# Kernel optimization log

Measured on AMD Instinct MI355X. Metric: run time of the kernel, lower is better.

## Reference

```python
import jax, jax.numpy as jnp
import numpy as np

B, CE = 2, 32
D, H, W = 12, 256, 256
PATCH = (5, 19, 19)
DWS = (1, 2, 2)            # patch_dws_fact
REAL = (5, 38, 38)          # patch_size * dws
STRIDE = (1, 9, 9)
OFF = (0, 2, 2)             # fixed random-crop offsets (max_random_crop=(0,5,5))
NPT = (8, 25, 25)           # nb_patches per dim after crop
HID = 256
EPS = 1e-6


def setup_inputs() -> dict:
    key = jax.random.key(0)
    k1, k2, k3, k4, k5 = jax.random.split(key, 5)
    gt = jax.random.randint(k1, (B, 1, D, H, W), 0, 50).astype(jnp.float32)
    affs = (jax.random.uniform(k2, (B, 3, D, H, W)) < 0.9).astype(jnp.float32)
    target = jnp.concatenate([gt, affs], axis=1)            # [B,4,D,H,W]
    pred = jax.random.normal(k3, (B, CE, D, H, W), dtype=jnp.float32)
    W1 = jax.random.normal(k4, (CE, HID), dtype=jnp.float32) * 0.1
    b1 = jnp.zeros((HID,), jnp.float32)
    W2 = jax.random.normal(k5, (HID, PATCH[0] * PATCH[1] * PATCH[2]), dtype=jnp.float32) * 0.05
    b2 = jnp.zeros((PATCH[0] * PATCH[1] * PATCH[2],), jnp.float32)
    return {"target": target, "pred": pred, "W1": W1, "b1": b1, "W2": W2, "b2": b2}


def _extract_patches(x, shp, strd, npt):
    # x: [N,C,D,H,W] -> [N*nd*nh*nw, C, *shp], torch-unfold ordering (N-major, then d,h,w)
    N, C = x.shape[:2]
    di = jnp.arange(npt[0])[:, None] * strd[0] + jnp.arange(shp[0])  # [nd,pd]
    hi = jnp.arange(npt[1])[:, None] * strd[1] + jnp.arange(shp[1])
    wi = jnp.arange(npt[2])[:, None] * strd[2] + jnp.arange(shp[2])
    p = x[:, :, di]                     # [N,C,nd,pd,H,W]
    p = p[:, :, :, :, hi]               # [N,C,nd,pd,nh,ph,W]
    p = p[:, :, :, :, :, :, wi]         # [N,C,nd,pd,nh,ph,nw,pw]
    p = jnp.transpose(p, (0, 2, 4, 6, 1, 3, 5, 7))
    return p.reshape(N * npt[0] * npt[1] * npt[2], C, *shp)


def _strided_centers(x, start, strd, npt):
    # shape-(1,1,1) patch extraction == strided slice, flattened in (N,d,h,w) order
    c = x[:, :, start[0]::strd[0], start[1]::strd[1], start[2]::strd[2]]
    c = c[:, :, :npt[0], :npt[1], :npt[2]]
    return jnp.transpose(c, (0, 2, 3, 4, 1))  # [N,nd,nh,nw,C]


def reference(target, pred, W1, b1, W2, b2):
    gt = target[:, :1]                                    # GT segmentation labels
    bmask = jnp.max(1.0 - target[:, 1:], axis=1, keepdims=True)  # boundary mask

    # crop_slice_targets with fixed offsets OFF
    gt_c = gt[:, :, OFF[0]:, OFF[1]:, OFF[2]:]
    gt_patches = _extract_patches(gt_c, REAL, STRIDE, NPT)  # [Np,1,5,38,38]
    Np = gt_patches.shape[0]

    # crop_slice_emb: start shifted by real_patch//2
    emb_start = tuple(o + r // 2 for o, r in zip(OFF, REAL))  # (2,21,21)
    centers = _strided_centers(gt, emb_start, STRIDE, NPT).reshape(Np)        # label at center
    on_bnd = _strided_centers(bmask, emb_start, STRIDE, NPT).reshape(Np)

    me_masks = (gt_patches != centers[:, None, None, None, None]).astype(jnp.float32)
    ignore = (gt_patches == 0).astype(jnp.float32)

    # MaxPool3d(kernel=stride=DWS): [Np,1,5,38,38] -> [Np,1,5,19,19]
    def pool(t):
        t = t.reshape(Np, 1, REAL[0] // DWS[0], DWS[0], PATCH[1], DWS[1], PATCH[2], DWS[2])
        return t.max(axis=(3, 5, 7))
    patch_targets = pool(me_masks)
    patch_ignore = pool(ignore) > 0

    valid = (centers != 0) & (on_bnd != 1.0)              # [Np]

    # pred embeddings: pred_dws_fact=1 so same crop/stride; 1x1x1 patches
    emb = _strided_centers(pred, emb_start, STRIDE, NPT).reshape(Np, CE)
    h = jax.nn.relu(emb @ W1 + b1)
    pred_patches = jax.nn.sigmoid(h @ W2 + b2).reshape(Np, 1, *PATCH)

    # exclusion of invalid patches == zeroing both operands in the Dice sums;
    # ignore-mask voxels are zeroed in pred and target as in the original
    m = (valid[:, None, None, None, None] & (~patch_ignore)).astype(jnp.float32)
    p = pred_patches * m
    t = patch_targets * m

    # SorensenDiceLoss (single channel): -2 * sum(p*t) / (sum(p^2)+sum(t^2))
    num = jnp.sum(p * t)
    den = jnp.sum(p * p) + jnp.sum(t * t)
    loss = -2.0 * num / jnp.maximum(den, EPS)
    return loss
```

## Files before the change

kernel.cpp:

```cpp
#include <hip/hip_runtime.h>

#define B_    2
#define CE_   32
#define D_    12
#define H_    256
#define W_    256
#define HW_   (H_*W_)
#define HID_  256
#define NPD   8
#define NPH   25
#define NPW   25
#define NP_   10000
#define PJ    1805
#define NTILE 113
#define JTP   114
#define MS_   16
#define MB_   157
#define NSLOT (MB_*64)

typedef __attribute__((ext_vector_type(8))) short s8v;
typedef __attribute__((ext_vector_type(4))) float f32x4;

__device__ __forceinline__ unsigned short f2bf(float f) {
    unsigned u = __float_as_uint(f);
    u += 0x7FFFu + ((u >> 16) & 1u);
    return (unsigned short)(u >> 16);
}

__device__ __forceinline__ void decompose_n(int n, int& b, int& pd, int& ph, int& pw) {
    b = n / (NPD*NPH*NPW);
    int r = n - b*(NPD*NPH*NPW);
    pd = r / (NPH*NPW);
    int r2 = r - pd*(NPH*NPW);
    ph = r2 / NPW;
    pw = r2 - ph*NPW;
}

__global__ __launch_bounds__(256) void k_stage(
    const float* __restrict__ W2, const float* __restrict__ b2,
    const float* __restrict__ target, const float* __restrict__ pred,
    const float* __restrict__ W1, const float* __restrict__ b1,
    unsigned short* __restrict__ W2t, int2* __restrict__ lut,
    unsigned short* __restrict__ M, unsigned short* __restrict__ hA,
    int2* __restrict__ meta, int* __restrict__ cnt)
{
    const int bx = blockIdx.x;
    const int t  = threadIdx.x;

    if (bx < 114) {
        __shared__ unsigned short tile[16][264];
        const int j0 = bx * 16;
        const int jj = t & 15, kb = t >> 4;
        #pragma unroll
        for (int ki = 0; ki < 16; ki++) {
            const int k = kb*16 + ki;
            const int j = j0 + jj;
            const float v = (j < PJ) ? W2[(size_t)k*PJ + j] : 0.f;
            tile[jj][k] = f2bf(v);
        }
        __syncthreads();
        const int jr = t >> 4, kc = t & 15;
        s8v a = *(const s8v*)&tile[jr][kc*16];
        s8v b = *(const s8v*)&tile[jr][kc*16+8];
        *(s8v*)&W2t[(size_t)(j0+jr)*HID_ + kc*16]     = a;
        *(s8v*)&W2t[(size_t)(j0+jr)*HID_ + kc*16 + 8] = b;
    } else if (bx == 114) {
        for (int i = t; i < JTP*16; i += 256) {
            int off = 0; float bj = 0.f;
            if (i < PJ) {
                const int dz = i/361, rj = i - dz*361;
                const int yy = rj/19, xx = rj - yy*19;
                off = dz*HW_ + yy*(2*W_) + xx*2;
                bj = b2[i];
            }
            lut[i] = make_int2(off, __float_as_int(bj));
        }
    } else if (bx < 1651) {
        __shared__ float rows[5][256];
        const int bx2 = bx - 115;
        const int bd = bx2 >> 6;
        const int h0 = (bx2 & 63) << 2;
        const int b  = bd / D_, d = bd - b*D_;
        const size_t gbase = ((size_t)(b*4*D_) + d)*HW_;
        #pragma unroll
        for (int r = 0; r < 5; r++) {
            int h = h0 + r; if (h > 255) h = 255;
            rows[r][t] = target[gbase + h*W_ + t];
        }
        __syncthreads();
        const int w1 = (t < 255) ? t+1 : 255;
        #pragma unroll
        for (int r = 0; r < 4; r++) {
            const float g00 = rows[r][t],   g01 = rows[r][w1];
            const float g10 = rows[r+1][t], g11 = rows[r+1][w1];
            const float mn = fminf(fminf(g00,g01), fminf(g10,g11));
            const float mx = fmaxf(fmaxf(g00,g01), fmaxf(g10,g11));
            M[(size_t)bd*HW_ + (h0+r)*W_ + t] = (unsigned short)(((int)mn << 8) | (int)mx);
        }
    } else {
        __shared__ float emb_s[64][36];
        __shared__ int   slot_s[64];
        const int pb = bx - 1651;
        const int n0 = pb * 64;
        {
            const int m = t & 63, cg = t >> 6;
            int n = n0 + m; if (n >= NP_) n = NP_-1;
            int b, pd, ph, pw; decompose_n(n, b, pd, ph, pw);
            const int dc = 2+pd, hc = 21+9*ph, wc = 21+9*pw;
            const size_t base = ((size_t)(b*CE_ + cg*8)*D_ + dc)*HW_ + (size_t)hc*W_ + wc;
            #pragma unroll
            for (int i = 0; i < 8; i++)
                emb_s[m][cg*8+i] = pred[base + (size_t)i*D_*HW_];
        }
        if (t < 64) {
            int n = n0 + t; const bool inb = (n < NP_); if (!inb) n = NP_-1;
            int b, pd, ph, pw; decompose_n(n, b, pd, ph, pw);
            const int dc = 2+pd, hc = 21+9*ph, wc = 21+9*pw;
            const size_t tb = ((size_t)(b*4)*D_ + dc)*HW_ + (size_t)hc*W_ + wc;
            const float ctr = target[tb];
            const float a1 = target[tb + (size_t)(1*D_*HW_)];
            const float a2 = target[tb + (size_t)(2*D_*HW_)];
            const float a3 = target[tb + (size_t)(3*D_*HW_)];
            const bool v = inb && (ctr!=0.f) && (a1!=0.f) && (a2!=0.f) && (a3!=0.f);
            const unsigned long long bal = __ballot(v);
            int base = 0;
            if (t == 0) base = atomicAdd(cnt, __popcll(bal));
            base = __shfl(base, 0);
            int s = -1;
            if (v) {
                s = base + (int)__popcll(bal & ((1ull << t) - 1ull));
                const int ci = (int)ctr;
                meta[s] = make_int2((b*D_+pd)*HW_ + (2+9*ph)*W_ + (2+9*pw),
                                    (ci<<8)|ci);
            }
            slot_s[t] = s;
        }
        __syncthreads();
        float wcol[CE_];
        #pragma unroll
        for (int i = 0; i < CE_; i++) wcol[i] = W1[(size_t)i*HID_ + t];
        const float bb = b1[t];
        const int kk = t>>5, quad = (t>>3)&3, e = t&7;
        for (int mm = 0; mm < 64; mm++) {
            const int s = slot_s[mm];
            if (s < 0) continue;
            float a = bb;
            #pragma unroll
            for (int cc = 0; cc < CE_; cc += 4) {
                const float4 ev = *(const float4*)&emb_s[mm][cc];
                a = fmaf(ev.x, wcol[cc+0], a);
                a = fmaf(ev.y, wcol[cc+1], a);
                a = fmaf(ev.z, wcol[cc+2], a);
                a = fmaf(ev.w, wcol[cc+3], a);
            }
            hA[(size_t)(((s>>4)*8+kk)*4+quad)*128 + (s&15)*8 + e] = f2bf(fmaxf(a, 0.f));
        }
    }
}

__global__ __launch_bounds__(256, 4) void k_main(
    const unsigned short* __restrict__ hA, const unsigned short* __restrict__ W2t,
    const int2* __restrict__ lut, const unsigned short* __restrict__ M,
    const int2* __restrict__ meta, const int* __restrict__ cnt,
    double* __restrict__ accs)
{
    __shared__ float red_s[4][3];
    const int tid  = threadIdx.x;
    const int wv   = tid >> 6;
    const int lane = tid & 63;
    const int quad = lane >> 4;
    const int l16  = lane & 15;
    const int jt0  = blockIdx.x * 2;
    const int ms   = blockIdx.y;
    const int nv   = *cnt;
    const int nmt  = (nv + 15) >> 4;

    s8v bfr0[8], bfr1[8];
    {
        const unsigned short* w0 = W2t + (size_t)(jt0*16 + l16)*HID_ + quad*8;
        const unsigned short* w1 = w0 + 16*HID_;
        #pragma unroll
        for (int kk = 0; kk < 8; kk++) {
            bfr0[kk] = *(const s8v*)(w0 + kk*32);
            bfr1[kk] = *(const s8v*)(w1 + kk*32);
        }
    }
    const int j0 = jt0*16 + l16, j1 = j0 + 16;
    const int2 lb0 = lut[j0], lb1 = lut[j1];
    const bool jok0 = (j0 < PJ), jok1 = (j1 < PJ);
    const float bj0 = __int_as_float(lb0.y), bj1 = __int_as_float(lb1.y);

    float num = 0.f, denp = 0.f, dent = 0.f;

    for (int mt = ms*4 + wv; mt < nmt; mt += MS_*4) {
        const unsigned short* arow = hA + (size_t)mt*4096 + quad*128 + l16*8;
        f32x4 a0 = {0.f,0.f,0.f,0.f}, a1 = {0.f,0.f,0.f,0.f};
        #pragma unroll
        for (int kk = 0; kk < 8; kk++) {
            const s8v af = *(const s8v*)(arow + kk*512);
            a0 = __builtin_amdgcn_mfma_f32_16x16x32_bf16(af, bfr0[kk], a0, 0, 0, 0);
            a1 = __builtin_amdgcn_mfma_f32_16x16x32_bf16(af, bfr1[kk], a1, 0, 0, 0);
        }
        #pragma unroll
        for (int r = 0; r < 4; r++) {
            const int p = mt*16 + quad*4 + r;
            const bool pok = (p < nv);
            const int2 md = meta[pok ? p : 0];
            const int mb = md.x;
            const unsigned cpv = (unsigned)md.y;
            if (pok) {
                if (jok0) {
                    const unsigned mv = M[mb + lb0.x];
                    if (mv >= 256u) {
                        const float tv = (mv != cpv) ? 1.f : 0.f;
                        const float pv = 1.f / (1.f + __expf(-(a0[r] + bj0)));
                        num  = fmaf(pv, tv, num);
                        denp = fmaf(pv, pv, denp);
                        dent += tv;
                    }
                }
                if (jok1) {
                    const unsigned mv = M[mb + lb1.x];
                    if (mv >= 256u) {
                        const float tv = (mv != cpv) ? 1.f : 0.f;
                        const float pv = 1.f / (1.f + __expf(-(a1[r] + bj1)));
                        num  = fmaf(pv, tv, num);
                        denp = fmaf(pv, pv, denp);
                        dent += tv;
                    }
                }
            }
        }
    }

    #pragma unroll
    for (int off = 32; off > 0; off >>= 1) {
        num  += __shfl_down(num,  off);
        denp += __shfl_down(denp, off);
        dent += __shfl_down(dent, off);
    }
    if (lane == 0) { red_s[wv][0] = num; red_s[wv][1] = denp; red_s[wv][2] = dent; }
    __syncthreads();
    if (tid == 0) {
        const float n_ = red_s[0][0]+red_s[1][0]+red_s[2][0]+red_s[3][0];
        const float p_ = red_s[0][1]+red_s[1][1]+red_s[2][1]+red_s[3][1];
        const float t_ = red_s[0][2]+red_s[1][2]+red_s[2][2]+red_s[3][2];
        const int slot = (blockIdx.x + blockIdx.y*57) & 31;
        atomicAdd(&accs[slot*4 + 0], (double)n_);
        atomicAdd(&accs[slot*4 + 1], (double)p_);
        atomicAdd(&accs[slot*4 + 2], (double)t_);
    }
}

__global__ void k_final(const double* __restrict__ accs, float* __restrict__ out) {
    double num = 0.0, den = 0.0;
    for (int s = 0; s < 32; s++) {
        num += accs[s*4 + 0];
        den += accs[s*4 + 1] + accs[s*4 + 2];
    }
    const double d = den > 1e-6 ? den : 1e-6;
    out[0] = (float)(-2.0 * num / d);
}

extern "C" void kernel_launch(void* const* d_in, const int* in_sizes, int n_in,
                              void* d_out, int out_size, void* d_ws, size_t ws_size,
                              hipStream_t stream) {
    const float* target = (const float*)d_in[0];
    const float* pred   = (const float*)d_in[1];
    const float* W1     = (const float*)d_in[2];
    const float* b1     = (const float*)d_in[3];
    const float* W2     = (const float*)d_in[4];
    const float* b2     = (const float*)d_in[5];
    float* out = (float*)d_out;

    char* ws = (char*)d_ws;
    double*         accs = (double*)ws;
    int*            cnt  = (int*)(ws + 1024);
    int2*           meta = (int2*)(ws + 1056);
    unsigned short* hA   = (unsigned short*)(ws + 81472);
    unsigned short* W2t  = (unsigned short*)(ws + 5226048);
    int2*           lut  = (int2*)(ws + 6159936);
    unsigned short* Mx   = (unsigned short*)(ws + 6174528);

    hipMemsetAsync(d_ws, 0, 1056, stream);
    hipLaunchKernelGGL(k_stage, dim3(1808),     dim3(256), 0, stream,
                       W2, b2, target, pred, W1, b1, W2t, lut, Mx, hA, meta, cnt);
    hipLaunchKernelGGL(k_main,  dim3(57, MS_),  dim3(256), 0, stream,
                       hA, W2t, lut, Mx, meta, cnt, accs);
    hipLaunchKernelGGL(k_final, dim3(1), dim3(1), 0, stream, accs, out);
}
```

Before: 313.9 us.

## Fuse final reduction into main kernel and reorder staging blocks

```diff
diff --git a/kernel.cpp b/kernel.cpp
--- a/kernel.cpp
+++ b/kernel.cpp
@@ -12,11 +12,9 @@
 #define NPW   25
 #define NP_   10000
 #define PJ    1805
-#define NTILE 113
 #define JTP   114
 #define MS_   16
-#define MB_   157
-#define NSLOT (MB_*64)
+#define PB_   313
 
 typedef __attribute__((ext_vector_type(8))) short s8v;
 typedef __attribute__((ext_vector_type(4))) float f32x4;
@@ -47,81 +45,30 @@
     const int bx = blockIdx.x;
     const int t  = threadIdx.x;
 
-    if (bx < 114) {
-        __shared__ unsigned short tile[16][264];
-        const int j0 = bx * 16;
-        const int jj = t & 15, kb = t >> 4;
-        #pragma unroll
-        for (int ki = 0; ki < 16; ki++) {
-            const int k = kb*16 + ki;
-            const int j = j0 + jj;
-            const float v = (j < PJ) ? W2[(size_t)k*PJ + j] : 0.f;
-            tile[jj][k] = f2bf(v);
-        }
-        __syncthreads();
-        const int jr = t >> 4, kc = t & 15;
-        s8v a = *(const s8v*)&tile[jr][kc*16];
-        s8v b = *(const s8v*)&tile[jr][kc*16+8];
-        *(s8v*)&W2t[(size_t)(j0+jr)*HID_ + kc*16]     = a;
-        *(s8v*)&W2t[(size_t)(j0+jr)*HID_ + kc*16 + 8] = b;
-    } else if (bx == 114) {
-        for (int i = t; i < JTP*16; i += 256) {
-            int off = 0; float bj = 0.f;
-            if (i < PJ) {
-                const int dz = i/361, rj = i - dz*361;
-                const int yy = rj/19, xx = rj - yy*19;
-                off = dz*HW_ + yy*(2*W_) + xx*2;
-                bj = b2[i];
-            }
-            lut[i] = make_int2(off, __float_as_int(bj));
-        }
-    } else if (bx < 1651) {
-        __shared__ float rows[5][256];
-        const int bx2 = bx - 115;
-        const int bd = bx2 >> 6;
-        const int h0 = (bx2 & 63) << 2;
-        const int b  = bd / D_, d = bd - b*D_;
-        const size_t gbase = ((size_t)(b*4*D_) + d)*HW_;
-        #pragma unroll
-        for (int r = 0; r < 5; r++) {
-            int h = h0 + r; if (h > 255) h = 255;
-            rows[r][t] = target[gbase + h*W_ + t];
-        }
-        __syncthreads();
-        const int w1 = (t < 255) ? t+1 : 255;
-        #pragma unroll
-        for (int r = 0; r < 4; r++) {
-            const float g00 = rows[r][t],   g01 = rows[r][w1];
-            const float g10 = rows[r+1][t], g11 = rows[r+1][w1];
-            const float mn = fminf(fminf(g00,g01), fminf(g10,g11));
-            const float mx = fmaxf(fmaxf(g00,g01), fmaxf(g10,g11));
-            M[(size_t)bd*HW_ + (h0+r)*W_ + t] = (unsigned short)(((int)mn << 8) | (int)mx);
-        }
-    } else {
-        __shared__ float emb_s[64][36];
-        __shared__ int   slot_s[64];
-        const int pb = bx - 1651;
-        const int n0 = pb * 64;
+    if (bx < PB_) {
+        __shared__ float emb_s[32][36];
+        __shared__ int   slot_s[32];
+        const int n0 = bx * 32;
         {
-            const int m = t & 63, cg = t >> 6;
+            const int m = t & 31, cg = t >> 5;
             int n = n0 + m; if (n >= NP_) n = NP_-1;
             int b, pd, ph, pw; decompose_n(n, b, pd, ph, pw);
             const int dc = 2+pd, hc = 21+9*ph, wc = 21+9*pw;
-            const size_t base = ((size_t)(b*CE_ + cg*8)*D_ + dc)*HW_ + (size_t)hc*W_ + wc;
+            const size_t base = ((size_t)(b*CE_ + cg*4)*D_ + dc)*HW_ + (size_t)hc*W_ + wc;
             #pragma unroll
-            for (int i = 0; i < 8; i++)
-                emb_s[m][cg*8+i] = pred[base + (size_t)i*D_*HW_];
-        }
-        if (t < 64) {
+            for (int i = 0; i < 4; i++)
+                emb_s[m][cg*4+i] = pred[base + (size_t)i*D_*HW_];
+        }
+        if (t < 32) {
             int n = n0 + t; const bool inb = (n < NP_); if (!inb) n = NP_-1;
             int b, pd, ph, pw; decompose_n(n, b, pd, ph, pw);
             const int dc = 2+pd, hc = 21+9*ph, wc = 21+9*pw;
             const size_t tb = ((size_t)(b*4)*D_ + dc)*HW_ + (size_t)hc*W_ + wc;
             const float ctr = target[tb];
-            const float a1 = target[tb + (size_t)(1*D_*HW_)];
-            const float a2 = target[tb + (size_t)(2*D_*HW_)];
-            const float a3 = target[tb + (size_t)(3*D_*HW_)];
-            const bool v = inb && (ctr!=0.f) && (a1!=0.f) && (a2!=0.f) && (a3!=0.f);
+            const float a1v = target[tb + (size_t)(1*D_*HW_)];
+            const float a2v = target[tb + (size_t)(2*D_*HW_)];
+            const float a3v = target[tb + (size_t)(3*D_*HW_)];
+            const bool v = inb && (ctr!=0.f) && (a1v!=0.f) && (a2v!=0.f) && (a3v!=0.f);
             const unsigned long long bal = __ballot(v);
             int base = 0;
             if (t == 0) base = atomicAdd(cnt, __popcll(bal));
@@ -141,7 +88,7 @@
         for (int i = 0; i < CE_; i++) wcol[i] = W1[(size_t)i*HID_ + t];
         const float bb = b1[t];
         const int kk = t>>5, quad = (t>>3)&3, e = t&7;
-        for (int mm = 0; mm < 64; mm++) {
+        for (int mm = 0; mm < 32; mm++) {
             const int s = slot_s[mm];
             if (s < 0) continue;
             float a = bb;
@@ -155,6 +102,56 @@
             }
             hA[(size_t)(((s>>4)*8+kk)*4+quad)*128 + (s&15)*8 + e] = f2bf(fmaxf(a, 0.f));
         }
+    } else if (bx < PB_ + JTP) {
+        __shared__ unsigned short tile[16][264];
+        const int j0 = (bx - PB_) * 16;
+        const int jj = t & 15, kb = t >> 4;
+        #pragma unroll
+        for (int ki = 0; ki < 16; ki++) {
+            const int k = kb*16 + ki;
+            const int j = j0 + jj;
+            const float v = (j < PJ) ? W2[(size_t)k*PJ + j] : 0.f;
+            tile[jj][k] = f2bf(v);
+        }
+        __syncthreads();
+        const int jr = t >> 4, kc = t & 15;
+        s8v a = *(const s8v*)&tile[jr][kc*16];
+        s8v b = *(const s8v*)&tile[jr][kc*16+8];
+        *(s8v*)&W2t[(size_t)(j0+jr)*HID_ + kc*16]     = a;
+        *(s8v*)&W2t[(size_t)(j0+jr)*HID_ + kc*16 + 8] = b;
+    } else if (bx == PB_ + JTP) {
+        for (int i = t; i < JTP*16; i += 256) {
+            int off = 0; float bj = 0.f;
+            if (i < PJ) {
+                const int dz = i/361, rj = i - dz*361;
+                const int yy = rj/19, xx = rj - yy*19;
+                off = dz*HW_ + yy*(2*W_) + xx*2;
+                bj = b2[i];
+            }
+            lut[i] = make_int2(off, __float_as_int(bj));
+        }
+    } else {
+        __shared__ float rows[9][256];
+        const int bx2 = bx - (PB_ + JTP + 1);
+        const int bd = bx2 >> 5;
+        const int h0 = (bx2 & 31) << 3;
+        const int b  = bd / D_, d = bd - b*D_;
+        const size_t gbase = ((size_t)(b*4*D_) + d)*HW_;
+        #pragma unroll
+        for (int r = 0; r < 9; r++) {
+            int h = h0 + r; if (h > 255) h = 255;
+            rows[r][t] = target[gbase + h*W_ + t];
+        }
+        __syncthreads();
+        const int w1 = (t < 255) ? t+1 : 255;
+        #pragma unroll
+        for (int r = 0; r < 8; r++) {
+            const float g00 = rows[r][t],   g01 = rows[r][w1];
+            const float g10 = rows[r+1][t], g11 = rows[r+1][w1];
+            const float mn = fminf(fminf(g00,g01), fminf(g10,g11));
+            const float mx = fmaxf(fmaxf(g00,g01), fmaxf(g10,g11));
+            M[(size_t)bd*HW_ + (h0+r)*W_ + t] = (unsigned short)(((int)mn << 8) | (int)mx);
+        }
     }
 }
 
@@ -162,7 +159,8 @@
     const unsigned short* __restrict__ hA, const unsigned short* __restrict__ W2t,
     const int2* __restrict__ lut, const unsigned short* __restrict__ M,
     const int2* __restrict__ meta, const int* __restrict__ cnt,
-    double* __restrict__ accs)
+    double* __restrict__ accs, unsigned* __restrict__ ticket,
+    float* __restrict__ out)
 {
     __shared__ float red_s[4][3];
     const int tid  = threadIdx.x;
@@ -189,8 +187,33 @@
     const int2 lb0 = lut[j0], lb1 = lut[j1];
     const bool jok0 = (j0 < PJ), jok1 = (j1 < PJ);
     const float bj0 = __int_as_float(lb0.y), bj1 = __int_as_float(lb1.y);
+    const unsigned short* Mp0 = M + lb0.x;
+    const unsigned short* Mp1 = M + lb1.x;
 
     float num = 0.f, denp = 0.f, dent = 0.f;
+
+#define EPI(MB, CPV) do {                                              \
+        if (jok0) {                                                    \
+            const unsigned mv = Mp0[(MB)];                             \
+            if (mv >= 256u) {                                          \
+                const float tv = (mv != (CPV)) ? 1.f : 0.f;            \
+                const float pv = 1.f / (1.f + __expf(-(a0[r] + bj0))); \
+                num  = fmaf(pv, tv, num);                              \
+                denp = fmaf(pv, pv, denp);                             \
+                dent += tv;                                            \
+            }                                                          \
+        }                                                              \
+        if (jok1) {                                                    \
+            const unsigned mv = Mp1[(MB)];                             \
+            if (mv >= 256u) {                                          \
+                const float tv = (mv != (CPV)) ? 1.f : 0.f;            \
+                const float pv = 1.f / (1.f + __expf(-(a1[r] + bj1))); \
+                num  = fmaf(pv, tv, num);                              \
+                denp = fmaf(pv, pv, denp);                             \
+                dent += tv;                                            \
+            }                                                          \
+        }                                                              \
+    } while (0)
 
     for (int mt = ms*4 + wv; mt < nmt; mt += MS_*4) {
         const unsigned short* arow = hA + (size_t)mt*4096 + quad*128 + l16*8;
@@ -201,37 +224,29 @@
             a0 = __builtin_amdgcn_mfma_f32_16x16x32_bf16(af, bfr0[kk], a0, 0, 0, 0);
             a1 = __builtin_amdgcn_mfma_f32_16x16x32_bf16(af, bfr1[kk], a1, 0, 0, 0);
         }
-        #pragma unroll
-        for (int r = 0; r < 4; r++) {
-            const int p = mt*16 + quad*4 + r;
-            const bool pok = (p < nv);
-            const int2 md = meta[pok ? p : 0];
-            const int mb = md.x;
-            const unsigned cpv = (unsigned)md.y;
-            if (pok) {
-                if (jok0) {
-                    const unsigned mv = M[mb + lb0.x];
-                    if (mv >= 256u) {
-                        const float tv = (mv != cpv) ? 1.f : 0.f;
-                        const float pv = 1.f / (1.f + __expf(-(a0[r] + bj0)));
-                        num  = fmaf(pv, tv, num);
-                        denp = fmaf(pv, pv, denp);
-                        dent += tv;
-                    }
-                }
-                if (jok1) {
-                    const unsigned mv = M[mb + lb1.x];
-                    if (mv >= 256u) {
-                        const float tv = (mv != cpv) ? 1.f : 0.f;
-                        const float pv = 1.f / (1.f + __expf(-(a1[r] + bj1)));
-                        num  = fmaf(pv, tv, num);
-                        denp = fmaf(pv, pv, denp);
-                        dent += tv;
-                    }
-                }
-            }
-        }
-    }
+        if (mt*16 + 16 <= nv) {
+            const int4* mp = (const int4*)(meta + mt*16 + quad*4);
+            const int4 u = mp[0], v = mp[1];
+            #pragma unroll
+            for (int r = 0; r < 4; r++) {
+                const int mb = (r==0) ? u.x : (r==1) ? u.z : (r==2) ? v.x : v.z;
+                const unsigned cpv = (unsigned)((r==0) ? u.y : (r==1) ? u.w
+                                                : (r==2) ? v.y : v.w);
+                EPI(mb, cpv);
+            }
+        } else {
+            #pragma unroll
+            for (int r = 0; r < 4; r++) {
+                const int p = mt*16 + quad*4 + r;
+                const bool pok = (p < nv);
+                const int2 md = meta[pok ? p : 0];
+                const int mb = md.x;
+                const unsigned cpv = (unsigned)md.y;
+                if (pok) { EPI(mb, cpv); }
+            }
+        }
+    }
+#undef EPI
 
     #pragma unroll
     for (int off = 32; off > 0; off >>= 1) {
@@ -249,17 +264,20 @@
         atomicAdd(&accs[slot*4 + 0], (double)n_);
         atomicAdd(&accs[slot*4 + 1], (double)p_);
         atomicAdd(&accs[slot*4 + 2], (double)t_);
-    }
-}
-
-__global__ void k_final(const double* __restrict__ accs, float* __restrict__ out) {
-    double num = 0.0, den = 0.0;
-    for (int s = 0; s < 32; s++) {
-        num += accs[s*4 + 0];
-        den += accs[s*4 + 1] + accs[s*4 + 2];
-    }
-    const double d = den > 1e-6 ? den : 1e-6;
-    out[0] = (float)(-2.0 * num / d);
+        __threadfence();
+        const unsigned done = atomicAdd(ticket, 1u);
+        if (done == gridDim.x * gridDim.y - 1u) {
+            __threadfence();
+            double nn = 0.0, dd = 0.0;
+            for (int s2 = 0; s2 < 32; s2++) {
+                nn += atomicAdd(&accs[s2*4 + 0], 0.0);
+                dd += atomicAdd(&accs[s2*4 + 1], 0.0)
+                    + atomicAdd(&accs[s2*4 + 2], 0.0);
+            }
+            const double d = dd > 1e-6 ? dd : 1e-6;
+            out[0] = (float)(-2.0 * nn / d);
+        }
+    }
 }
 
 extern "C" void kernel_launch(void* const* d_in, const int* in_sizes, int n_in,
@@ -274,18 +292,18 @@
     float* out = (float*)d_out;
 
     char* ws = (char*)d_ws;
-    double*         accs = (double*)ws;
-    int*            cnt  = (int*)(ws + 1024);
-    int2*           meta = (int2*)(ws + 1056);
-    unsigned short* hA   = (unsigned short*)(ws + 81472);
-    unsigned short* W2t  = (unsigned short*)(ws + 5226048);
-    int2*           lut  = (int2*)(ws + 6159936);
-    unsigned short* Mx   = (unsigned short*)(ws + 6174528);
+    double*         accs   = (double*)ws;
+    int*            cnt    = (int*)(ws + 1024);
+    unsigned*       ticket = (unsigned*)(ws + 1028);
+    int2*           meta   = (int2*)(ws + 1056);
+    unsigned short* hA     = (unsigned short*)(ws + 81472);
+    unsigned short* W2t    = (unsigned short*)(ws + 5226048);
+    int2*           lut    = (int2*)(ws + 6159936);
+    unsigned short* Mx     = (unsigned short*)(ws + 6174528);
 
     hipMemsetAsync(d_ws, 0, 1056, stream);
-    hipLaunchKernelGGL(k_stage, dim3(1808),     dim3(256), 0, stream,
+    hipLaunchKernelGGL(k_stage, dim3(1196),    dim3(256), 0, stream,
                        W2, b2, target, pred, W1, b1, W2t, lut, Mx, hA, meta, cnt);
-    hipLaunchKernelGGL(k_main,  dim3(57, MS_),  dim3(256), 0, stream,
-                       hA, W2t, lut, Mx, meta, cnt, accs);
-    hipLaunchKernelGGL(k_final, dim3(1), dim3(1), 0, stream, accs, out);
-}
+    hipLaunchKernelGGL(k_main,  dim3(57, MS_), dim3(256), 0, stream,
+                       hA, W2t, lut, Mx, meta, cnt, accs, ticket, out);
+}
```

Result: slower. 357.1 us (+13.8%).
